# Optimization experiments

Measured on AMD Instinct MI355X. Metric: run time of the kernel, lower is better.

The kernel has to match this reference:

```python
import jax, jax.numpy as jnp
import numpy as np

QMIN_A, QMAX_A = -128, 127   # int8 activation range
QMIN_W, QMAX_W = -8, 7       # int4 weight range
EPS = float(np.finfo(np.float32).eps)


def per_token_dynamic_quant(x):
    """Asymmetric per-token int8 quantize -> dequantize (fake quant), matching torchao."""
    mn = jnp.minimum(jnp.min(x, axis=-1, keepdims=True), 0.0)
    mx = jnp.maximum(jnp.max(x, axis=-1, keepdims=True), 0.0)
    scale = jnp.maximum((mx - mn) / (QMAX_A - QMIN_A), EPS)
    zp = jnp.clip(QMIN_A - jnp.round(mn / scale), QMIN_A, QMAX_A)
    q = jnp.clip(jnp.round(x / scale) + zp, QMIN_A, QMAX_A)
    return (q - zp) * scale


def setup_inputs() -> dict:
    key = jax.random.key(0)
    k1, k2, k3, k4 = jax.random.split(key, 4)
    B, S, IN, OUT, G = 4, 2048, 4096, 4096, 256
    x = jax.random.normal(k1, (B, S, IN), dtype=jnp.float32)
    # int4 values stored in int8 container, range [-8, 7]
    weight_int8 = jax.random.randint(k2, (OUT, IN), QMIN_W, QMAX_W + 1, dtype=jnp.int32).astype(jnp.int8)
    scales = jax.random.uniform(k3, (OUT, IN // G), dtype=jnp.float32, minval=0.005, maxval=0.02)
    zeros = jnp.round(jax.random.uniform(k4, (OUT, IN // G), minval=-2.0, maxval=2.0)).astype(jnp.float32)
    bias = jax.random.normal(jax.random.fold_in(key, 7), (OUT,), dtype=jnp.float32) * 0.01
    return {"x": x, "weight_int8": weight_int8, "scales": scales, "zeros": zeros, "bias": bias}


def reference(x, weight_int8, scales, zeros, bias):
    O, I = weight_int8.shape
    G = I // scales.shape[1]
    xq = per_token_dynamic_quant(x)
    # groupwise int4 dequant: (w - zero_point) * scale per (1, G) block
    w = weight_int8.astype(jnp.float32).reshape(O, I // G, G)
    w_dq = ((w - zeros[:, :, None]) * scales[:, :, None]).reshape(O, I)
    return jnp.einsum('bsi,oi->bso', xq, w_dq) + bias
```

## Files before the change

kernel.cpp:

```cpp
#include <hip/hip_runtime.h>
#include <stdint.h>

typedef __attribute__((ext_vector_type(4))) int   i32x4;
typedef __attribute__((ext_vector_type(16))) int  i32x16;

#define TM 256
#define TN 128
#define BKB 128
#define NSTAGE 3


__device__ __forceinline__ void async16(const void* g, void* l) {
  __builtin_amdgcn_global_load_lds(
      (__attribute__((address_space(1))) void*)g,
      (__attribute__((address_space(3))) void*)l,
      16, 0, 0);
}

__device__ __forceinline__ int swz(int r) { return (r ^ (r >> 3)) & 7; }

__global__ __launch_bounds__(256) void prep_kernel(
    const float* __restrict__ x, int8_t* __restrict__ Aq,
    float* __restrict__ tokScale, float* __restrict__ tokZp,
    const int* __restrict__ W, const float* __restrict__ scales,
    const float* __restrict__ zeros, int8_t* __restrict__ Wq,
    float* __restrict__ T, int K, int M, int gpr, int G)
{
  const int t = threadIdx.x;
  const int wave = t >> 6, lane = t & 63;
  __shared__ float sA[4], sB[4];

  if ((int)blockIdx.x < M) {
    const int token = blockIdx.x;
    const float4* xin = (const float4*)(x + (size_t)token * K);
    float4 v[4];
#pragma unroll
    for (int j = 0; j < 4; ++j) v[j] = xin[t + 256 * j];

    float mn = v[0].x, mx = v[0].x;
#pragma unroll
    for (int j = 0; j < 4; ++j) {
      mn = fminf(mn, fminf(fminf(v[j].x, v[j].y), fminf(v[j].z, v[j].w)));
      mx = fmaxf(mx, fmaxf(fmaxf(v[j].x, v[j].y), fmaxf(v[j].z, v[j].w)));
    }
#pragma unroll
    for (int off = 32; off >= 1; off >>= 1) {
      mn = fminf(mn, __shfl_xor(mn, off));
      mx = fmaxf(mx, __shfl_xor(mx, off));
    }
    if (lane == 0) { sA[wave] = mn; sB[wave] = mx; }
    __syncthreads();
    mn = fminf(fminf(sA[0], sA[1]), fminf(sA[2], sA[3]));
    mx = fmaxf(fmaxf(sB[0], sB[1]), fmaxf(sB[2], sB[3]));

    mn = fminf(mn, 0.0f);
    mx = fmaxf(mx, 0.0f);
    const float scale = fmaxf((mx - mn) / 255.0f, 1.1920929e-07f);
    float zp = -128.0f - rintf(mn / scale);
    zp = fminf(fmaxf(zp, -128.0f), 127.0f);
    const float rs = 1.0f / scale;

    uint32_t* dst = (uint32_t*)(Aq + (size_t)token * K);
#pragma unroll
    for (int j = 0; j < 4; ++j) {
      float e[4] = {v[j].x, v[j].y, v[j].z, v[j].w};
      uint32_t pk = 0;
#pragma unroll
      for (int i = 0; i < 4; ++i) {
        float q = rintf(e[i] * rs) + zp;
        q = fminf(fmaxf(q, -128.0f), 127.0f);
        pk |= ((uint32_t)(int)q & 0xFFu) << (8 * i);
      }
      dst[t + 256 * j] = pk;
    }
    if (t == 0) { tokScale[token] = scale; tokZp[token] = zp; }
  } else {
    const int row = blockIdx.x - M;
    const int4* wp = (const int4*)(W + (size_t)row * K);
    uint32_t* dst = (uint32_t*)(Wq + (size_t)row * K);

    float partial = 0.0f;
#pragma unroll
    for (int j = 0; j < 4; ++j) {
      const int idx = t + 256 * j;
      const int g = (idx * 4) / G;
      const float s = scales[(size_t)row * gpr + g];
      const int zi = (int)zeros[(size_t)row * gpr + g];
      int4 w4 = wp[idx];
      const int a = w4.x - zi, b = w4.y - zi, c = w4.z - zi, d = w4.w - zi;
      dst[idx] = ((uint32_t)a & 0xFFu) | (((uint32_t)b & 0xFFu) << 8)
               | (((uint32_t)c & 0xFFu) << 16) | (((uint32_t)d & 0xFFu) << 24);
      partial += s * (float)(a + b + c + d);
    }
#pragma unroll
    for (int off = 32; off >= 1; off >>= 1) partial += __shfl_xor(partial, off);
    if (lane == 0) sA[wave] = partial;
    __syncthreads();
    if (t == 0) T[row] = (sA[0] + sA[1]) + (sA[2] + sA[3]);
  }
}

__global__ __launch_bounds__(512, 2) void gemm_kernel(
    const int8_t* __restrict__ A,
    const int8_t* __restrict__ B,
    const float* __restrict__ scales,
    const float* __restrict__ tokScale, const float* __restrict__ tokZp,
    const float* __restrict__ T, const float* __restrict__ bias,
    float* __restrict__ C, int M, int N, int K, int gpr)
{
  __shared__ __align__(16) int8_t As[NSTAGE][TM * BKB];
  __shared__ __align__(16) int8_t Bs[NSTAGE][TN * BKB];
  __shared__ float sS[16 * TN];

  const int tid   = threadIdx.x;
  const int lane  = tid & 63;
  const int wave  = tid >> 6;
  const int m0 = blockIdx.y * TM;
  const int n0 = blockIdx.x * TN;
  const int wm = (wave & 3) * 64;
  const int wn = (wave >> 2) * 64;
  const int col32 = lane & 31;
  const int khalf = lane >> 5;

  int rAoff[2], kA[2], rBoff[2], kB[2];
#pragma unroll
  for (int i = 0; i < 2; ++i) {
    const int rA = wm + i * 32 + col32; rAoff[i] = rA * BKB; kA[i] = swz(rA);
    const int rB = wn + i * 32 + col32; rBoff[i] = rB * BKB; kB[i] = swz(rB);
  }

  const int8_t* aSrc[4]; int aLds[4];
  const int8_t* bSrc[2]; int bLds[2];
#pragma unroll
  for (int it = 0; it < 4; ++it) {
    const int p = (it << 9) | tid;
    const int r = p >> 3;
    const int c = (p & 7) ^ swz(r);
    aSrc[it] = A + (size_t)(m0 + r) * K + (c << 4);
    aLds[it] = it * 8192 + wave * 1024;
  }
#pragma unroll
  for (int it = 0; it < 2; ++it) {
    const int p = (it << 9) | tid;
    const int r = p >> 3;
    const int c = (p & 7) ^ swz(r);
    bSrc[it] = B + (size_t)(n0 + r) * K + (c << 4);
    bLds[it] = it * 8192 + wave * 1024;
  }

#pragma unroll
  for (int jj = 0; jj < (16 * TN) / 512; ++jj) {
    const int flat = tid + 512 * jj;
    const int i = flat >> 4, g = flat & 15;
    sS[g * TN + i] = scales[(size_t)(n0 + i) * gpr + g];
  }

  float accf[2][2][16];
#pragma unroll
  for (int i = 0; i < 2; ++i)
#pragma unroll
    for (int j = 0; j < 2; ++j)
#pragma unroll
      for (int r = 0; r < 16; ++r) accf[i][j][r] = 0.0f;

  i32x16 zeroC;
#pragma unroll
  for (int r = 0; r < 16; ++r) zeroC[r] = 0;
  i32x16 ai[2][2];

  const int nsteps = K / BKB;
  const int ngroups = nsteps / 2;

#define STAGE(sb, tt) do {                                                   \
    const size_t koff = (size_t)(tt) * BKB;                                  \
    _Pragma("unroll")                                                        \
    for (int it = 0; it < 4; ++it) async16(aSrc[it] + koff, &As[sb][aLds[it]]); \
    _Pragma("unroll")                                                        \
    for (int it = 0; it < 2; ++it) async16(bSrc[it] + koff, &Bs[sb][bLds[it]]); \
  } while (0)

#define COMPUTE(sb, FIRST) do {                                              \
    __builtin_amdgcn_s_setprio(1);                                           \
    _Pragma("unroll")                                                        \
    for (int kk = 0; kk < 4; ++kk) {                                         \
      const int cw = kk * 2 + khalf;                                         \
      i32x4 af[2], bf[2];                                                    \
      _Pragma("unroll")                                                      \
      for (int i = 0; i < 2; ++i)                                            \
        af[i] = *(const i32x4*)&As[sb][rAoff[i] + ((cw ^ kA[i]) << 4)];      \
      _Pragma("unroll")                                                      \
      for (int j = 0; j < 2; ++j)                                            \
        bf[j] = *(const i32x4*)&Bs[sb][rBoff[j] + ((cw ^ kB[j]) << 4)];      \
      _Pragma("unroll")                                                      \
      for (int i = 0; i < 2; ++i)                                            \
        _Pragma("unroll")                                                    \
        for (int j = 0; j < 2; ++j) {                                        \
          if (FIRST && kk == 0)                                              \
            ai[i][j] = __builtin_amdgcn_mfma_i32_32x32x32_i8(af[i], bf[j], zeroC, 0, 0, 0); \
          else                                                               \
            ai[i][j] = __builtin_amdgcn_mfma_i32_32x32x32_i8(af[i], bf[j], ai[i][j], 0, 0, 0); \
        }                                                                    \
    }                                                                        \
    __builtin_amdgcn_s_setprio(0);                                           \
  } while (0)

#define FIXUP(g) do {                                                        \
    _Pragma("unroll")                                                        \
    for (int j = 0; j < 2; ++j) {                                            \
      const float s = sS[(g) * TN + wn + j * 32 + col32];                    \
      _Pragma("unroll")                                                      \
      for (int i = 0; i < 2; ++i)                                            \
        _Pragma("unroll")                                                    \
        for (int r = 0; r < 16; ++r)                                         \
          accf[i][j][r] += s * (float)ai[i][j][r];                           \
    }                                                                        \
  } while (0)

#define SYNC6() do { asm volatile("s_waitcnt vmcnt(6) lgkmcnt(0)" ::: "memory"); \
                     __builtin_amdgcn_s_barrier(); } while (0)
#define SYNC0() do { asm volatile("s_waitcnt vmcnt(0) lgkmcnt(0)" ::: "memory"); \
                     __builtin_amdgcn_s_barrier(); } while (0)

  STAGE(0, 0);
  STAGE(1, 1);
  asm volatile("s_waitcnt vmcnt(6) lgkmcnt(0)" ::: "memory");
  __builtin_amdgcn_s_barrier();

  int b0 = 0, b1 = 1, b2 = 2;
  for (int g = 0; g < ngroups; ++g) {
    const int t = 2 * g;
    if (t + 2 < nsteps) { STAGE(b2, t + 2); COMPUTE(b0, true); SYNC6(); }
    else                {                   COMPUTE(b0, true); SYNC0(); }
    if (t + 3 < nsteps)      { STAGE(b0, t + 3); COMPUTE(b1, false); FIXUP(g); SYNC6(); }
    else if (t + 2 < nsteps) {                   COMPUTE(b1, false); FIXUP(g); SYNC0(); }
    else                     {                   COMPUTE(b1, false); FIXUP(g); }
    const int tmp = b0; b0 = b2; b2 = b1; b1 = tmp;
  }

#undef STAGE
#undef COMPUTE
#undef FIXUP
#undef SYNC6
#undef SYNC0

  int   nj[2];
  float Tn[2], bn[2];
#pragma unroll
  for (int j = 0; j < 2; ++j) {
    nj[j] = n0 + wn + j * 32 + col32;
    Tn[j] = T[nj[j]];
    bn[j] = bias[nj[j]];
  }
  const int rbase = 4 * khalf;
#pragma unroll
  for (int i = 0; i < 2; ++i) {
    const int mb = m0 + wm + i * 32;
#pragma unroll
    for (int r = 0; r < 16; ++r) {
      const int m = mb + (r & 3) + 8 * (r >> 2) + rbase;
      const float ts = tokScale[m];
      const float zp = tokZp[m];
      float* crow = C + (size_t)m * N;
#pragma unroll
      for (int j = 0; j < 2; ++j)
        crow[nj[j]] = ts * (accf[i][j][r] - zp * Tn[j]) + bn[j];
    }
  }
}

extern "C" void kernel_launch(void* const* d_in, const int* in_sizes, int n_in,
                              void* d_out, int out_size, void* d_ws, size_t ws_size,
                              hipStream_t stream) {
  const float* x      = (const float*)d_in[0];
  const int*   w      = (const int*)d_in[1];
  const float* scales = (const float*)d_in[2];
  const float* zeros  = (const float*)d_in[3];
  const float* bias   = (const float*)d_in[4];
  float* out = (float*)d_out;

  const int OUT = in_sizes[4];
  const int IN  = in_sizes[1] / OUT;
  const int M   = in_sizes[0] / IN;
  const int gpr = in_sizes[2] / OUT;
  const int G   = IN / gpr;

  int8_t* Aq = (int8_t*)d_ws;
  int8_t* Wq = Aq + (size_t)M * IN;
  float* tokScale = (float*)(Wq + (size_t)OUT * IN);
  float* tokZp = tokScale + M;
  float* T = tokZp + M;

  prep_kernel<<<M + OUT, 256, 0, stream>>>(x, Aq, tokScale, tokZp,
                                           w, scales, zeros, Wq, T, IN, M, gpr, G);
  gemm_kernel<<<dim3(OUT / TN, M / TM), 512, 0, stream>>>(
      Aq, Wq, scales, tokScale, tokZp, T, bias, out, M, OUT, IN, gpr);
}
```

Baseline: 459.8 us.

## Interleave async global-to-LDS loads with MFMA phases and per-phase barriers

Splits each k-step into four phases. Each phase issues its LDS fragment reads, then one slice of the next stage's global_load_lds copies, then a barrier and lgkmcnt wait, then four MFMAs under raised priority, in the style of a ping-pong schedule. The goal is to spread memory issue across the compute and keep waves in lockstep so LDS reads and MFMAs overlap better. In exchange it adds several extra s_barriers per k-step, and the FIXUP loops lose their explicit unroll pragmas, which could cost sync overhead or scheduling quality.

Measured after the change: 492.5 us. +7.1%, slower.

```diff
diff --git a/kernel.cpp b/kernel.cpp
--- a/kernel.cpp
+++ b/kernel.cpp
@@ -171,77 +171,104 @@
   const int nsteps = K / BKB;
   const int ngroups = nsteps / 2;
 
-#define STAGE(sb, tt) do {                                                   \
-    const size_t koff = (size_t)(tt) * BKB;                                  \
-    _Pragma("unroll")                                                        \
-    for (int it = 0; it < 4; ++it) async16(aSrc[it] + koff, &As[sb][aLds[it]]); \
-    _Pragma("unroll")                                                        \
-    for (int it = 0; it < 2; ++it) async16(bSrc[it] + koff, &Bs[sb][bLds[it]]); \
+#define PH(sb, kk, FIRST, STG, ENDW) do {                                      \
+    const int cw = (kk) * 2 + khalf;                                           \
+    const i32x4 af0 = *(const i32x4*)&As[sb][rAoff[0] + ((cw ^ kA[0]) << 4)];  \
+    const i32x4 af1 = *(const i32x4*)&As[sb][rAoff[1] + ((cw ^ kA[1]) << 4)];  \
+    const i32x4 bf0 = *(const i32x4*)&Bs[sb][rBoff[0] + ((cw ^ kB[0]) << 4)];  \
+    const i32x4 bf1 = *(const i32x4*)&Bs[sb][rBoff[1] + ((cw ^ kB[1]) << 4)];  \
+    STG;                                                                       \
+    __builtin_amdgcn_s_barrier();                                              \
+    asm volatile("s_waitcnt lgkmcnt(0)" ::: "memory");                         \
+    __builtin_amdgcn_sched_barrier(0);                                         \
+    __builtin_amdgcn_s_setprio(1);                                             \
+    if (FIRST) {                                                               \
+      ai[0][0] = __builtin_amdgcn_mfma_i32_32x32x32_i8(af0, bf0, zeroC, 0,0,0);\
+      ai[0][1] = __builtin_amdgcn_mfma_i32_32x32x32_i8(af0, bf1, zeroC, 0,0,0);\
+      ai[1][0] = __builtin_amdgcn_mfma_i32_32x32x32_i8(af1, bf0, zeroC, 0,0,0);\
+      ai[1][1] = __builtin_amdgcn_mfma_i32_32x32x32_i8(af1, bf1, zeroC, 0,0,0);\
+    } else {                                                                   \
+      ai[0][0] = __builtin_amdgcn_mfma_i32_32x32x32_i8(af0, bf0, ai[0][0], 0,0,0);\
+      ai[0][1] = __builtin_amdgcn_mfma_i32_32x32x32_i8(af0, bf1, ai[0][1], 0,0,0);\
+      ai[1][0] = __builtin_amdgcn_mfma_i32_32x32x32_i8(af1, bf0, ai[1][0], 0,0,0);\
+      ai[1][1] = __builtin_amdgcn_mfma_i32_32x32x32_i8(af1, bf1, ai[1][1], 0,0,0);\
+    }                                                                          \
+    __builtin_amdgcn_s_setprio(0);                                             \
+    ENDW;                                                                      \
   } while (0)
 
-#define COMPUTE(sb, FIRST) do {                                              \
-    __builtin_amdgcn_s_setprio(1);                                           \
-    _Pragma("unroll")                                                        \
-    for (int kk = 0; kk < 4; ++kk) {                                         \
-      const int cw = kk * 2 + khalf;                                         \
-      i32x4 af[2], bf[2];                                                    \
-      _Pragma("unroll")                                                      \
-      for (int i = 0; i < 2; ++i)                                            \
-        af[i] = *(const i32x4*)&As[sb][rAoff[i] + ((cw ^ kA[i]) << 4)];      \
-      _Pragma("unroll")                                                      \
-      for (int j = 0; j < 2; ++j)                                            \
-        bf[j] = *(const i32x4*)&Bs[sb][rBoff[j] + ((cw ^ kB[j]) << 4)];      \
-      _Pragma("unroll")                                                      \
-      for (int i = 0; i < 2; ++i)                                            \
-        _Pragma("unroll")                                                    \
-        for (int j = 0; j < 2; ++j) {                                        \
-          if (FIRST && kk == 0)                                              \
-            ai[i][j] = __builtin_amdgcn_mfma_i32_32x32x32_i8(af[i], bf[j], zeroC, 0, 0, 0); \
-          else                                                               \
-            ai[i][j] = __builtin_amdgcn_mfma_i32_32x32x32_i8(af[i], bf[j], ai[i][j], 0, 0, 0); \
-        }                                                                    \
-    }                                                                        \
-    __builtin_amdgcn_s_setprio(0);                                           \
+#define SA2(i0, i1, pb, tt) do {                                               \
+    async16(aSrc[i0] + (size_t)(tt) * BKB, &As[pb][aLds[i0]]);                 \
+    async16(aSrc[i1] + (size_t)(tt) * BKB, &As[pb][aLds[i1]]); } while (0)
+#define SB1(i0, pb, tt)                                                        \
+    async16(bSrc[i0] + (size_t)(tt) * BKB, &Bs[pb][bLds[i0]])
+#define NOSTG do {} while (0)
+
+#define FIXUP(gg) do {                                                         \
+    for (int j = 0; j < 2; ++j) {                                              \
+      const float s = sS[(gg) * TN + wn + j * 32 + col32];                     \
+      for (int i = 0; i < 2; ++i)                                              \
+        for (int r = 0; r < 16; ++r)                                           \
+          accf[i][j][r] += s * (float)ai[i][j][r];                             \
+    }                                                                          \
   } while (0)
 
-#define FIXUP(g) do {                                                        \
-    _Pragma("unroll")                                                        \
-    for (int j = 0; j < 2; ++j) {                                            \
-      const float s = sS[(g) * TN + wn + j * 32 + col32];                    \
-      _Pragma("unroll")                                                      \
-      for (int i = 0; i < 2; ++i)                                            \
-        _Pragma("unroll")                                                    \
-        for (int r = 0; r < 16; ++r)                                         \
-          accf[i][j][r] += s * (float)ai[i][j][r];                           \
-    }                                                                        \
+#define BARO  __builtin_amdgcn_s_barrier()
+#define T6    do { asm volatile("s_waitcnt vmcnt(6)" ::: "memory");            \
+                   __builtin_amdgcn_s_barrier(); } while (0)
+#define T0    do { asm volatile("s_waitcnt vmcnt(0)" ::: "memory");            \
+                   __builtin_amdgcn_s_barrier(); } while (0)
+#define T6F(gg) do { FIXUP(gg);                                                \
+                   asm volatile("s_waitcnt vmcnt(6)" ::: "memory");            \
+                   __builtin_amdgcn_s_barrier(); } while (0)
+#define TEND(gg) FIXUP(gg)
+
+#define STEP_S(sb, pb, tt, FIRST, TAIL) do {                                   \
+    PH(sb, 0, FIRST, SA2(0, 1, pb, tt), BARO);                                 \
+    PH(sb, 1, false, SA2(2, 3, pb, tt), BARO);                                 \
+    PH(sb, 2, false, SB1(0, pb, tt),    BARO);                                 \
+    PH(sb, 3, false, SB1(1, pb, tt),    TAIL);                                 \
   } while (0)
-
-#define SYNC6() do { asm volatile("s_waitcnt vmcnt(6) lgkmcnt(0)" ::: "memory"); \
-                     __builtin_amdgcn_s_barrier(); } while (0)
-#define SYNC0() do { asm volatile("s_waitcnt vmcnt(0) lgkmcnt(0)" ::: "memory"); \
-                     __builtin_amdgcn_s_barrier(); } while (0)
-
-  STAGE(0, 0);
-  STAGE(1, 1);
+#define STEP_N(sb, FIRST, TAIL) do {                                           \
+    PH(sb, 0, FIRST, NOSTG, BARO);                                             \
+    PH(sb, 1, false, NOSTG, BARO);                                             \
+    PH(sb, 2, false, NOSTG, BARO);                                             \
+    PH(sb, 3, false, NOSTG, TAIL);                                             \
+  } while (0)
+
+#pragma unroll
+  for (int it = 0; it < 4; ++it) async16(aSrc[it], &As[0][aLds[it]]);
+#pragma unroll
+  for (int it = 0; it < 2; ++it) async16(bSrc[it], &Bs[0][bLds[it]]);
+#pragma unroll
+  for (int it = 0; it < 4; ++it) async16(aSrc[it] + BKB, &As[1][aLds[it]]);
+#pragma unroll
+  for (int it = 0; it < 2; ++it) async16(bSrc[it] + BKB, &Bs[1][bLds[it]]);
   asm volatile("s_waitcnt vmcnt(6) lgkmcnt(0)" ::: "memory");
   __builtin_amdgcn_s_barrier();
 
   int b0 = 0, b1 = 1, b2 = 2;
   for (int g = 0; g < ngroups; ++g) {
     const int t = 2 * g;
-    if (t + 2 < nsteps) { STAGE(b2, t + 2); COMPUTE(b0, true); SYNC6(); }
-    else                {                   COMPUTE(b0, true); SYNC0(); }
-    if (t + 3 < nsteps)      { STAGE(b0, t + 3); COMPUTE(b1, false); FIXUP(g); SYNC6(); }
-    else if (t + 2 < nsteps) {                   COMPUTE(b1, false); FIXUP(g); SYNC0(); }
-    else                     {                   COMPUTE(b1, false); FIXUP(g); }
+    if (t + 2 < nsteps) STEP_S(b0, b2, t + 2, true, T6);
+    else                STEP_N(b0, true, T0);
+    if (t + 3 < nsteps) STEP_S(b1, b0, t + 3, false, T6F(g));
+    else                STEP_N(b1, false, TEND(g));
     const int tmp = b0; b0 = b2; b2 = b1; b1 = tmp;
   }
 
-#undef STAGE
-#undef COMPUTE
+#undef PH
+#undef SA2
+#undef SB1
+#undef NOSTG
 #undef FIXUP
-#undef SYNC6
-#undef SYNC0
+#undef BARO
+#undef T6
+#undef T0
+#undef T6F
+#undef TEND
+#undef STEP_S
+#undef STEP_N
 
   int   nj[2];
   float Tn[2], bn[2];
```
